# Kernel optimization log

Hardware: AMD Instinct MI355X
Metric: run time of the kernel (lower is better)

The kernel has to match this reference:

```python
import jax, jax.numpy as jnp
import numpy as np

# (multiplicity, irrep dimension 2l+1) for irreps_in == irreps_out == 128x0e+128x1o+128x2e
IRREPS = [(128, 1), (128, 3), (128, 5)]
N_NODES = 100000
DIM = sum(m * d for m, d in IRREPS)  # 1152
W_NUMEL = sum(m * m for m, _ in IRREPS)  # 49152
B_NUMEL = IRREPS[0][0]  # bias only on scalar 0e irrep -> 128


def setup_inputs() -> dict:
    key = jax.random.key(0)
    k1, k2, k3 = jax.random.split(key, 3)
    x = jax.random.normal(k1, (N_NODES, DIM), dtype=jnp.float32)
    w = jax.random.normal(k2, (W_NUMEL,), dtype=jnp.float32)
    b = jax.random.normal(k3, (B_NUMEL,), dtype=jnp.float32)
    return {"x": x, "w": w, "b": b}


def reference(x, w, b):
    # Segmented tensor-product linear: one small (mul_in x mul_out) matmul per irrep
    # segment, scaled by path_weight = (sum of contributing mul_in)^-0.5 = 128^-0.5,
    # then bias (path_weight 1.0) added only on the scalar 0e output slice.
    outs = []
    off_x = 0
    off_w = 0
    for idx, (mul, d) in enumerate(IRREPS):
        seg = x[:, off_x:off_x + mul * d].reshape(-1, mul, d)  # [N, mul, 2l+1]
        W = w[off_w:off_w + mul * mul].reshape(mul, mul)       # [mul_in, mul_out]
        pw = 1.0 / np.sqrt(mul)                                # element normalization
        o = pw * jnp.einsum('nui,uv->nvi', seg, W)             # [N, mul, 2l+1]
        if idx == 0:
            o = o + b.reshape(mul, d)                          # bias on scalars only
        outs.append(o.reshape(-1, mul * d))
        off_x += mul * d
        off_w += mul * mul
    return jnp.concatenate(outs, axis=-1)  # [N, DIM]
```

## Files before the change

### kernel.cpp

```cpp
#include <hip/hip_runtime.h>

typedef __attribute__((ext_vector_type(8))) short bf16x8;
typedef __attribute__((ext_vector_type(4))) float f32x4;

#define NBLK   16
#define DIMF   1152
#define NTILE  6250
#define GRIDSZ 512
#define ROWU   1160

static __device__ __forceinline__ unsigned short f2bf(float f) {
    unsigned int u = __builtin_bit_cast(unsigned int, f);
    return (unsigned short)((u + 0x7FFFu + ((u >> 16) & 1u)) >> 16);
}

__global__ __launch_bounds__(512, 2)
void seglin_kernel(const float* __restrict__ x, const float* __restrict__ w,
                   const float* __restrict__ b, float* __restrict__ out) {
    __shared__ unsigned short xs[2][NBLK][ROWU];

    const int tid  = threadIdx.x;
    const int wv   = tid >> 6;
    const int lane = tid & 63;
    const int lq   = lane & 15;
    const int lg   = lane >> 4;
    const int v0   = wv * 16;

    const int sn = tid >> 5;
    const int st = tid & 31;

    const float pw = 0.08838834764831845f;

    bf16x8 wf[3][4];
    const int woff[3] = {0, 16384, 32768};
    #pragma unroll
    for (int s = 0; s < 3; ++s)
        #pragma unroll
        for (int t = 0; t < 4; ++t) {
            bf16x8 f;
            #pragma unroll
            for (int e = 0; e < 8; ++e) {
                int u = 32 * t + lg * 8 + e;
                f[e] = (short)f2bf(pw * w[woff[s] + u * 128 + v0 + lq]);
            }
            wf[s][t] = f;
        }

    float biasr[4];
    #pragma unroll
    for (int e = 0; e < 4; ++e) biasr[e] = b[v0 + lg * 4 + e];

    float4 g0, g1[3], g2[5];

#define STAGE_LOAD(TILE) do {                                                   \
        const float* src = x + ((long)(TILE) * NBLK + sn) * DIMF;               \
        g0    = *reinterpret_cast<const float4*>(src + 4 * st);                 \
        g1[0] = *reinterpret_cast<const float4*>(src + 128 + 12 * st);          \
        g1[1] = *reinterpret_cast<const float4*>(src + 128 + 12 * st + 4);      \
        g1[2] = *reinterpret_cast<const float4*>(src + 128 + 12 * st + 8);      \
        g2[0] = *reinterpret_cast<const float4*>(src + 512 + 20 * st);          \
        g2[1] = *reinterpret_cast<const float4*>(src + 512 + 20 * st + 4);      \
        g2[2] = *reinterpret_cast<const float4*>(src + 512 + 20 * st + 8);      \
        g2[3] = *reinterpret_cast<const float4*>(src + 512 + 20 * st + 12);     \
        g2[4] = *reinterpret_cast<const float4*>(src + 512 + 20 * st + 16);     \
    } while (0)

#define STAGE_WRITE(BUF) do {                                                   \
        unsigned short* dst = &xs[BUF][sn][0];                                  \
        { ushort4 h;                                                            \
          h.x = f2bf(g0.x); h.y = f2bf(g0.y); h.z = f2bf(g0.z); h.w = f2bf(g0.w); \
          *reinterpret_cast<ushort4*>(dst + 4 * st) = h; }                      \
        float f1[12], f2[20];                                                   \
        f1[0]=g1[0].x; f1[1]=g1[0].y; f1[2]=g1[0].z; f1[3]=g1[0].w;             \
        f1[4]=g1[1].x; f1[5]=g1[1].y; f1[6]=g1[1].z; f1[7]=g1[1].w;             \
        f1[8]=g1[2].x; f1[9]=g1[2].y; f1[10]=g1[2].z; f1[11]=g1[2].w;           \
        _Pragma("unroll")                                                       \
        for (int i = 0; i < 3; ++i) {                                           \
            ushort4 h;                                                          \
            h.x = f2bf(f1[0 + i]); h.y = f2bf(f1[3 + i]);                       \
            h.z = f2bf(f1[6 + i]); h.w = f2bf(f1[9 + i]);                       \
            *reinterpret_cast<ushort4*>(dst + 128 + (i << 7) + 4 * st) = h;     \
        }                                                                       \
        f2[0]=g2[0].x; f2[1]=g2[0].y; f2[2]=g2[0].z; f2[3]=g2[0].w;             \
        f2[4]=g2[1].x; f2[5]=g2[1].y; f2[6]=g2[1].z; f2[7]=g2[1].w;             \
        f2[8]=g2[2].x; f2[9]=g2[2].y; f2[10]=g2[2].z; f2[11]=g2[2].w;           \
        f2[12]=g2[3].x; f2[13]=g2[3].y; f2[14]=g2[3].z; f2[15]=g2[3].w;         \
        f2[16]=g2[4].x; f2[17]=g2[4].y; f2[18]=g2[4].z; f2[19]=g2[4].w;         \
        _Pragma("unroll")                                                       \
        for (int i = 0; i < 5; ++i) {                                           \
            ushort4 h;                                                          \
            h.x = f2bf(f2[0 + i]);  h.y = f2bf(f2[5 + i]);                      \
            h.z = f2bf(f2[10 + i]); h.w = f2bf(f2[15 + i]);                     \
            *reinterpret_cast<ushort4*>(dst + 512 + (i << 7) + 4 * st) = h;     \
        }                                                                       \
    } while (0)

    long tile = blockIdx.x;
    STAGE_LOAD(tile);
    STAGE_WRITE(0);
    __syncthreads();

    int cur = 0;
    for (; tile < NTILE; tile += GRIDSZ) {
        const bool has_next = (tile + GRIDSZ) < NTILE;

        if (has_next) STAGE_LOAD(tile + GRIDSZ);

        const unsigned short* row = &xs[cur][lq][0];
        float* orow = out + (tile * NBLK + lq) * (long)DIMF;
        const int vb = v0 + lg * 4;

        {
            f32x4 a0 = {0.f, 0.f, 0.f, 0.f};
            #pragma unroll
            for (int t = 0; t < 4; ++t) {
                bf16x8 bf = *reinterpret_cast<const bf16x8*>(row + 32 * t + lg * 8);
                a0 = __builtin_amdgcn_mfma_f32_16x16x32_bf16(wf[0][t], bf, a0, 0, 0, 0);
            }
            float4 o0;
            o0.x = a0[0] + biasr[0];
            o0.y = a0[1] + biasr[1];
            o0.z = a0[2] + biasr[2];
            o0.w = a0[3] + biasr[3];
            *reinterpret_cast<float4*>(orow + vb) = o0;
        }

        {
            f32x4 aB[3];
            #pragma unroll
            for (int j = 0; j < 3; ++j) { f32x4 z = {0.f,0.f,0.f,0.f}; aB[j] = z; }
            #pragma unroll
            for (int t = 0; t < 4; ++t) {
                const int u0 = 32 * t + lg * 8;
                #pragma unroll
                for (int j = 0; j < 3; ++j) {
                    bf16x8 bf = *reinterpret_cast<const bf16x8*>(row + ((1 + j) << 7) + u0);
                    aB[j] = __builtin_amdgcn_mfma_f32_16x16x32_bf16(wf[1][t], bf, aB[j], 0, 0, 0);
                }
            }
            float* p1o = orow + 128 + 3 * vb;
            #pragma unroll
            for (int k = 0; k < 3; ++k) {
                float4 o;
                o.x = aB[(4 * k + 0) % 3][(4 * k + 0) / 3];
                o.y = aB[(4 * k + 1) % 3][(4 * k + 1) / 3];
                o.z = aB[(4 * k + 2) % 3][(4 * k + 2) / 3];
                o.w = aB[(4 * k + 3) % 3][(4 * k + 3) / 3];
                *reinterpret_cast<float4*>(p1o + 4 * k) = o;
            }
        }

        {
            f32x4 aC[5];
            #pragma unroll
            for (int j = 0; j < 5; ++j) { f32x4 z = {0.f,0.f,0.f,0.f}; aC[j] = z; }
            #pragma unroll
            for (int t = 0; t < 4; ++t) {
                const int u0 = 32 * t + lg * 8;
                #pragma unroll
                for (int j = 0; j < 5; ++j) {
                    bf16x8 bf = *reinterpret_cast<const bf16x8*>(row + ((4 + j) << 7) + u0);
                    aC[j] = __builtin_amdgcn_mfma_f32_16x16x32_bf16(wf[2][t], bf, aC[j], 0, 0, 0);
                }
            }
            float* p2o = orow + 512 + 5 * vb;
            #pragma unroll
            for (int k = 0; k < 5; ++k) {
                float4 o;
                o.x = aC[(4 * k + 0) % 5][(4 * k + 0) / 5];
                o.y = aC[(4 * k + 1) % 5][(4 * k + 1) / 5];
                o.z = aC[(4 * k + 2) % 5][(4 * k + 2) / 5];
                o.w = aC[(4 * k + 3) % 5][(4 * k + 3) / 5];
                *reinterpret_cast<float4*>(p2o + 4 * k) = o;
            }
        }

        if (has_next) STAGE_WRITE(cur ^ 1);

        asm volatile("s_waitcnt lgkmcnt(0)\n\ts_barrier" ::: "memory");
        cur ^= 1;
    }
#undef STAGE_LOAD
#undef STAGE_WRITE
}

extern "C" void kernel_launch(void* const* d_in, const int* in_sizes, int n_in,
                              void* d_out, int out_size, void* d_ws, size_t ws_size,
                              hipStream_t stream) {
    const float* x = (const float*)d_in[0];
    const float* w = (const float*)d_in[1];
    const float* b = (const float*)d_in[2];
    float* outp = (float*)d_out;
    seglin_kernel<<<dim3(GRIDSZ), dim3(512), 0, stream>>>(x, w, b, outp);
}
```

Baseline: 187.4 us.

## Split next-tile prefetch into two halves and raise occupancy to four blocks

The global-to-LDS prefetch of the next tile is split into two phases: the 0e/1o part is loaded at loop start and written mid-iteration, while the 2e part is loaded after the 1o MFMAs and written at the end. This shortens how long prefetched registers stay live, and launch_bounds is raised to ask for four 512-thread blocks per CU. LDS use (about 74 KB per block) likely still caps residency, so the higher occupancy target may only force register spills without adding blocks. The later 2e load also gives that load less time to hide under compute.

```diff
diff --git a/kernel.cpp b/kernel.cpp
--- a/kernel.cpp
+++ b/kernel.cpp
@@ -14,7 +14,7 @@
     return (unsigned short)((u + 0x7FFFu + ((u >> 16) & 1u)) >> 16);
 }
 
-__global__ __launch_bounds__(512, 2)
+__global__ __launch_bounds__(512, 4)
 void seglin_kernel(const float* __restrict__ x, const float* __restrict__ w,
                    const float* __restrict__ b, float* __restrict__ out) {
     __shared__ unsigned short xs[2][NBLK][ROWU];
@@ -50,14 +50,19 @@
     #pragma unroll
     for (int e = 0; e < 4; ++e) biasr[e] = b[v0 + lg * 4 + e];
 
-    float4 g0, g1[3], g2[5];
-
-#define STAGE_LOAD(TILE) do {                                                   \
+    float4 g0, g1[3];
+    float4 g2[5];
+
+#define STAGE_LOAD_H1(TILE) do {                                                \
         const float* src = x + ((long)(TILE) * NBLK + sn) * DIMF;               \
         g0    = *reinterpret_cast<const float4*>(src + 4 * st);                 \
         g1[0] = *reinterpret_cast<const float4*>(src + 128 + 12 * st);          \
         g1[1] = *reinterpret_cast<const float4*>(src + 128 + 12 * st + 4);      \
         g1[2] = *reinterpret_cast<const float4*>(src + 128 + 12 * st + 8);      \
+    } while (0)
+
+#define STAGE_LOAD_H2(TILE) do {                                                \
+        const float* src = x + ((long)(TILE) * NBLK + sn) * DIMF;               \
         g2[0] = *reinterpret_cast<const float4*>(src + 512 + 20 * st);          \
         g2[1] = *reinterpret_cast<const float4*>(src + 512 + 20 * st + 4);      \
         g2[2] = *reinterpret_cast<const float4*>(src + 512 + 20 * st + 8);      \
@@ -65,12 +70,12 @@
         g2[4] = *reinterpret_cast<const float4*>(src + 512 + 20 * st + 16);     \
     } while (0)
 
-#define STAGE_WRITE(BUF) do {                                                   \
+#define STAGE_WRITE_H1(BUF) do {                                                \
         unsigned short* dst = &xs[BUF][sn][0];                                  \
         { ushort4 h;                                                            \
           h.x = f2bf(g0.x); h.y = f2bf(g0.y); h.z = f2bf(g0.z); h.w = f2bf(g0.w); \
           *reinterpret_cast<ushort4*>(dst + 4 * st) = h; }                      \
-        float f1[12], f2[20];                                                   \
+        float f1[12];                                                           \
         f1[0]=g1[0].x; f1[1]=g1[0].y; f1[2]=g1[0].z; f1[3]=g1[0].w;             \
         f1[4]=g1[1].x; f1[5]=g1[1].y; f1[6]=g1[1].z; f1[7]=g1[1].w;             \
         f1[8]=g1[2].x; f1[9]=g1[2].y; f1[10]=g1[2].z; f1[11]=g1[2].w;           \
@@ -81,6 +86,11 @@
             h.z = f2bf(f1[6 + i]); h.w = f2bf(f1[9 + i]);                       \
             *reinterpret_cast<ushort4*>(dst + 128 + (i << 7) + 4 * st) = h;     \
         }                                                                       \
+    } while (0)
+
+#define STAGE_WRITE_H2(BUF) do {                                                \
+        unsigned short* dst = &xs[BUF][sn][0];                                  \
+        float f2[20];                                                           \
         f2[0]=g2[0].x; f2[1]=g2[0].y; f2[2]=g2[0].z; f2[3]=g2[0].w;             \
         f2[4]=g2[1].x; f2[5]=g2[1].y; f2[6]=g2[1].z; f2[7]=g2[1].w;             \
         f2[8]=g2[2].x; f2[9]=g2[2].y; f2[10]=g2[2].z; f2[11]=g2[2].w;           \
@@ -96,15 +106,17 @@
     } while (0)
 
     long tile = blockIdx.x;
-    STAGE_LOAD(tile);
-    STAGE_WRITE(0);
+    STAGE_LOAD_H1(tile);
+    STAGE_WRITE_H1(0);
+    STAGE_LOAD_H2(tile);
+    STAGE_WRITE_H2(0);
     __syncthreads();
 
     int cur = 0;
     for (; tile < NTILE; tile += GRIDSZ) {
         const bool has_next = (tile + GRIDSZ) < NTILE;
 
-        if (has_next) STAGE_LOAD(tile + GRIDSZ);
+        if (has_next) STAGE_LOAD_H1(tile + GRIDSZ);
 
         const unsigned short* row = &xs[cur][lq][0];
         float* orow = out + (tile * NBLK + lq) * (long)DIMF;
@@ -150,6 +162,11 @@
             }
         }
 
+        if (has_next) {
+            STAGE_WRITE_H1(cur ^ 1);
+            STAGE_LOAD_H2(tile + GRIDSZ);
+        }
+
         {
             f32x4 aC[5];
             #pragma unroll
@@ -175,13 +192,15 @@
             }
         }
 
-        if (has_next) STAGE_WRITE(cur ^ 1);
+        if (has_next) STAGE_WRITE_H2(cur ^ 1);
 
         asm volatile("s_waitcnt lgkmcnt(0)\n\ts_barrier" ::: "memory");
         cur ^= 1;
     }
-#undef STAGE_LOAD
-#undef STAGE_WRITE
+#undef STAGE_LOAD_H1
+#undef STAGE_LOAD_H2
+#undef STAGE_WRITE_H1
+#undef STAGE_WRITE_H2
 }
 
 extern "C" void kernel_launch(void* const* d_in, const int* in_sizes, int n_in,
```

Result: slower. 264.7 us (+41.3%).

## Prepack bf16 weight fragments in a prep kernel and reload per tile for occupancy

Applied to the files above, without the earlier changes.

A separate prep kernel scales the weights, converts them to bf16 and stores them into a fragment-ordered workspace buffer. The main kernel no longer keeps all weight fragments resident in registers across the loop. Instead it reloads them with 16-byte vector loads at the start of each tile, which frees registers so launch bounds can ask for 4 blocks per CU instead of 2. The LDS row padding also changes from 1160 to 1168 elements to alter the bank mapping. In exchange there is an extra kernel launch and repeated weight reads (likely cache hits) every tile, and LDS use of about 74 KB per block may cap how many blocks actually fit on a CU.

```diff
diff --git a/kernel.cpp b/kernel.cpp
--- a/kernel.cpp
+++ b/kernel.cpp
@@ -7,15 +7,29 @@
 #define DIMF   1152
 #define NTILE  6250
 #define GRIDSZ 512
-#define ROWU   1160
+#define ROWU   1168
+#define WNUM   49152
 
 static __device__ __forceinline__ unsigned short f2bf(float f) {
     unsigned int u = __builtin_bit_cast(unsigned int, f);
     return (unsigned short)((u + 0x7FFFu + ((u >> 16) & 1u)) >> 16);
 }
 
-__global__ __launch_bounds__(512, 2)
-void seglin_kernel(const float* __restrict__ x, const float* __restrict__ w,
+__global__ __launch_bounds__(256)
+void prep_w(const float* __restrict__ w, unsigned short* __restrict__ wb) {
+    int d = blockIdx.x * 256 + threadIdx.x;
+    if (d >= WNUM) return;
+    int e  = d & 7;
+    int v  = (d >> 3) & 127;
+    int lg = (d >> 10) & 3;
+    int t  = (d >> 12) & 3;
+    int s  = d >> 14;
+    int u  = 32 * t + 8 * lg + e;
+    wb[d] = f2bf(0.08838834764831845f * w[s * 16384 + u * 128 + v]);
+}
+
+__global__ __launch_bounds__(512, 4)
+void seglin_kernel(const float* __restrict__ x, const unsigned short* __restrict__ wb,
                    const float* __restrict__ b, float* __restrict__ out) {
     __shared__ unsigned short xs[2][NBLK][ROWU];
 
@@ -29,22 +43,7 @@
     const int sn = tid >> 5;
     const int st = tid & 31;
 
-    const float pw = 0.08838834764831845f;
-
-    bf16x8 wf[3][4];
-    const int woff[3] = {0, 16384, 32768};
-    #pragma unroll
-    for (int s = 0; s < 3; ++s)
-        #pragma unroll
-        for (int t = 0; t < 4; ++t) {
-            bf16x8 f;
-            #pragma unroll
-            for (int e = 0; e < 8; ++e) {
-                int u = 32 * t + lg * 8 + e;
-                f[e] = (short)f2bf(pw * w[woff[s] + u * 128 + v0 + lq]);
-            }
-            wf[s][t] = f;
-        }
+    const int fbase = (lg << 10) + ((v0 + lq) << 3);
 
     float biasr[4];
     #pragma unroll
@@ -70,7 +69,7 @@
         { ushort4 h;                                                            \
           h.x = f2bf(g0.x); h.y = f2bf(g0.y); h.z = f2bf(g0.z); h.w = f2bf(g0.w); \
           *reinterpret_cast<ushort4*>(dst + 4 * st) = h; }                      \
-        float f1[12], f2[20];                                                   \
+        float f1[12];                                                           \
         f1[0]=g1[0].x; f1[1]=g1[0].y; f1[2]=g1[0].z; f1[3]=g1[0].w;             \
         f1[4]=g1[1].x; f1[5]=g1[1].y; f1[6]=g1[1].z; f1[7]=g1[1].w;             \
         f1[8]=g1[2].x; f1[9]=g1[2].y; f1[10]=g1[2].z; f1[11]=g1[2].w;           \
@@ -81,6 +80,7 @@
             h.z = f2bf(f1[6 + i]); h.w = f2bf(f1[9 + i]);                       \
             *reinterpret_cast<ushort4*>(dst + 128 + (i << 7) + 4 * st) = h;     \
         }                                                                       \
+        float f2[20];                                                           \
         f2[0]=g2[0].x; f2[1]=g2[0].y; f2[2]=g2[0].z; f2[3]=g2[0].w;             \
         f2[4]=g2[1].x; f2[5]=g2[1].y; f2[6]=g2[1].z; f2[7]=g2[1].w;             \
         f2[8]=g2[2].x; f2[9]=g2[2].y; f2[10]=g2[2].z; f2[11]=g2[2].w;           \
@@ -104,6 +104,14 @@
     for (; tile < NTILE; tile += GRIDSZ) {
         const bool has_next = (tile + GRIDSZ) < NTILE;
 
+        bf16x8 af[3][4];
+        #pragma unroll
+        for (int s = 0; s < 3; ++s)
+            #pragma unroll
+            for (int t = 0; t < 4; ++t)
+                af[s][t] = *reinterpret_cast<const bf16x8*>(
+                    wb + (((s * 4 + t) << 12) + fbase));
+
         if (has_next) STAGE_LOAD(tile + GRIDSZ);
 
         const unsigned short* row = &xs[cur][lq][0];
@@ -115,7 +123,7 @@
             #pragma unroll
             for (int t = 0; t < 4; ++t) {
                 bf16x8 bf = *reinterpret_cast<const bf16x8*>(row + 32 * t + lg * 8);
-                a0 = __builtin_amdgcn_mfma_f32_16x16x32_bf16(wf[0][t], bf, a0, 0, 0, 0);
+                a0 = __builtin_amdgcn_mfma_f32_16x16x32_bf16(af[0][t], bf, a0, 0, 0, 0);
             }
             float4 o0;
             o0.x = a0[0] + biasr[0];
@@ -135,7 +143,7 @@
                 #pragma unroll
                 for (int j = 0; j < 3; ++j) {
                     bf16x8 bf = *reinterpret_cast<const bf16x8*>(row + ((1 + j) << 7) + u0);
-                    aB[j] = __builtin_amdgcn_mfma_f32_16x16x32_bf16(wf[1][t], bf, aB[j], 0, 0, 0);
+                    aB[j] = __builtin_amdgcn_mfma_f32_16x16x32_bf16(af[1][t], bf, aB[j], 0, 0, 0);
                 }
             }
             float* p1o = orow + 128 + 3 * vb;
@@ -160,7 +168,7 @@
                 #pragma unroll
                 for (int j = 0; j < 5; ++j) {
                     bf16x8 bf = *reinterpret_cast<const bf16x8*>(row + ((4 + j) << 7) + u0);
-                    aC[j] = __builtin_amdgcn_mfma_f32_16x16x32_bf16(wf[2][t], bf, aC[j], 0, 0, 0);
+                    aC[j] = __builtin_amdgcn_mfma_f32_16x16x32_bf16(af[2][t], bf, aC[j], 0, 0, 0);
                 }
             }
             float* p2o = orow + 512 + 5 * vb;
@@ -191,5 +199,8 @@
     const float* w = (const float*)d_in[1];
     const float* b = (const float*)d_in[2];
     float* outp = (float*)d_out;
-    seglin_kernel<<<dim3(GRIDSZ), dim3(512), 0, stream>>>(x, w, b, outp);
-}
+    unsigned short* wb = (unsigned short*)d_ws;
+
+    prep_w<<<dim3((WNUM + 255) / 256), dim3(256), 0, stream>>>(w, wb);
+    seglin_kernel<<<dim3(GRIDSZ), dim3(512), 0, stream>>>(x, wb, b, outp);
+}
```

Measured after the change: 258.7 us. 1.38x slower.
